# Kernel optimization log

Hardware: AMD Instinct MI355X
Metric: run time of the kernel (lower is better)

The kernel has to match this reference:

```python
import jax, jax.numpy as jnp
import numpy as np

N_NODES = 50000
N_EDGES = 800000
IN_FEATS = 128
OUT_FEATS = 64


def setup_inputs() -> dict:
    key = jax.random.key(0)
    k1, k2, k3, k4, k5, k6 = jax.random.split(key, 6)
    feat = jax.random.normal(k1, (N_NODES, IN_FEATS), dtype=jnp.float32)
    edge_src = jax.random.randint(k2, (N_EDGES,), 0, N_NODES, dtype=jnp.int64)
    edge_dst = jax.random.randint(k3, (N_EDGES,), 0, N_NODES, dtype=jnp.int64)
    eweight = jax.random.uniform(k4, (N_EDGES,), dtype=jnp.float32)
    W = jax.random.normal(k5, (OUT_FEATS, IN_FEATS), dtype=jnp.float32) * (1.0 / np.sqrt(IN_FEATS))
    b = jax.random.normal(k6, (OUT_FEATS,), dtype=jnp.float32) * 0.01
    return {"feat": feat, "edge_src": edge_src, "edge_dst": edge_dst,
            "eweight": eweight, "W": W, "b": b}


def reference(feat, edge_src, edge_dst, eweight, W, b):
    # Linear: [N, in] @ [in, out] + [out]
    h = jnp.einsum('ni,oi->no', feat, W) + b
    # u_mul_e: gather src features, scale by per-edge weight -> [E, out]
    m = h[edge_src] * eweight[:, None]
    # sum reduce over dst -> [N, out]
    out = jax.ops.segment_sum(m, edge_dst, num_segments=N_NODES)
    return out
```

## Files before the change

kernel.cpp:

```cpp
#include <hip/hip_runtime.h>

#define IN_FEATS 128
#define OUT_FEATS 64
#define TM 64
#define ALD 136
#define BW_LOG 6
#define BWIDTH 64
#define MAX_NB 1024
#define SE_PER_BLK 2048
#define CAP 2048
#define MAXR 4

typedef short bf16x8 __attribute__((ext_vector_type(8)));
typedef float f32x4 __attribute__((ext_vector_type(4)));

__device__ inline unsigned short f2bf(float f) {
    unsigned u = __float_as_uint(f);
    u += 0x7FFFu + ((u >> 16) & 1u);
    return (unsigned short)(u >> 16);
}
__device__ inline float bf2f_lo(unsigned v) { return __uint_as_float(v << 16); }
__device__ inline float bf2f_hi(unsigned v) { return __uint_as_float(v & 0xFFFF0000u); }
__device__ inline ushort4 cvt4(float4 t) {
    ushort4 s; s.x = f2bf(t.x); s.y = f2bf(t.y); s.z = f2bf(t.z); s.w = f2bf(t.w);
    return s;
}

__global__ __launch_bounds__(256) void init_cursors(int* __restrict__ gcur, int nb)
{
    for (int i = threadIdx.x; i < nb; i += 256) gcur[i] = 0;
}

__global__ __launch_bounds__(256) void stage_linear(
    const float* __restrict__ feat, const float* __restrict__ W,
    const float* __restrict__ b, unsigned short* __restrict__ h,
    const int* __restrict__ esrc, const int* __restrict__ edst,
    const float* __restrict__ ew, int* __restrict__ gcur,
    int2* __restrict__ gstage, int n_nodes, int n_edges, int nb, int nstage)
{
    __shared__ union {
        struct { unsigned short Ws[OUT_FEATS * ALD]; } lin;
        struct { int cnt[MAX_NB]; int base[MAX_NB]; } st;
    } sm;
    const int tid = threadIdx.x;

    if ((int)blockIdx.x < nstage) {
        int* cnt  = sm.st.cnt;
        int* base = sm.st.base;
        for (int i = tid; i < nb; i += 256) cnt[i] = 0;
        __syncthreads();

        const int e0 = blockIdx.x * SE_PER_BLK + tid * 8;
        int dk[8]; int sk[8]; float wk[8]; int bk[8]; int rk[8];
        if (e0 + 7 < n_edges) {
            *((int4*)&dk[0]) = *((const int4*)&edst[e0]);
            *((int4*)&dk[4]) = *((const int4*)&edst[e0 + 4]);
            *((int4*)&sk[0]) = *((const int4*)&esrc[e0]);
            *((int4*)&sk[4]) = *((const int4*)&esrc[e0 + 4]);
            *((float4*)&wk[0]) = *((const float4*)&ew[e0]);
            *((float4*)&wk[4]) = *((const float4*)&ew[e0 + 4]);
#pragma unroll
            for (int i = 0; i < 8; ++i) {
                bk[i] = dk[i] >> BW_LOG;
                rk[i] = atomicAdd(&cnt[bk[i]], 1);
            }
        } else {
#pragma unroll
            for (int i = 0; i < 8; ++i) {
                int e = e0 + i;
                if (e < n_edges) {
                    dk[i] = edst[e]; sk[i] = esrc[e]; wk[i] = ew[e];
                    bk[i] = dk[i] >> BW_LOG;
                    rk[i] = atomicAdd(&cnt[bk[i]], 1);
                } else bk[i] = -1;
            }
        }
        __syncthreads();
        for (int i = tid; i < nb; i += 256) {
            int c = cnt[i];
            base[i] = c ? atomicAdd(&gcur[i], c) : 0;
        }
        __syncthreads();
#pragma unroll
        for (int i = 0; i < 8; ++i) {
            if (bk[i] >= 0) {
                int off = base[bk[i]] + rk[i];
                if (off < CAP)
                    gstage[bk[i] * CAP + off] =
                        make_int2(((dk[i] & (BWIDTH - 1)) << 16) | sk[i],
                                  __float_as_int(wk[i]));
            }
        }
    } else {
        unsigned short* Ws = sm.lin.Ws;
        const int row0 = ((int)blockIdx.x - nstage) * TM;

        {
            const int c  = tid & 63;
            const int kb = (tid >> 6) * 32;
            const float4* wrow = (const float4*)(W + (size_t)c * IN_FEATS + kb);
#pragma unroll
            for (int i = 0; i < 8; ++i)
                *((ushort4*)&Ws[c * ALD + kb + i * 4]) = cvt4(wrow[i]);
        }
        __syncthreads();

        const int w    = tid >> 6;
        const int lane = tid & 63;
        const int m    = lane & 15;
        const int quad = lane >> 4;
        const int koff = quad * 8;

        const int gr = row0 + w * 16 + m;
        const bool rv = gr < n_nodes;
        const float* arow = feat + (size_t)gr * IN_FEATS;

        bf16x8 af[4];
        if (rv) {
            float4 t[8];
#pragma unroll
            for (int c = 0; c < 4; ++c) {
                t[2 * c]     = *((const float4*)(arow + c * 32 + koff));
                t[2 * c + 1] = *((const float4*)(arow + c * 32 + koff + 4));
            }
#pragma unroll
            for (int c = 0; c < 4; ++c) {
                ushort4 s0 = cvt4(t[2 * c]);
                ushort4 s1 = cvt4(t[2 * c + 1]);
                af[c] = (bf16x8){(short)s0.x, (short)s0.y, (short)s0.z, (short)s0.w,
                                 (short)s1.x, (short)s1.y, (short)s1.z, (short)s1.w};
            }
        } else {
#pragma unroll
            for (int c = 0; c < 4; ++c)
                af[c] = (bf16x8){0, 0, 0, 0, 0, 0, 0, 0};
        }

        f32x4 acc[4];
#pragma unroll
        for (int t = 0; t < 4; ++t) acc[t] = (f32x4){0.f, 0.f, 0.f, 0.f};

#pragma unroll
        for (int chunk = 0; chunk < 4; ++chunk) {
            const int kc = chunk * 32 + koff;
#pragma unroll
            for (int t = 0; t < 4; ++t) {
                bf16x8 bfr = *((const bf16x8*)&Ws[(t * 16 + m) * ALD + kc]);
                acc[t] = __builtin_amdgcn_mfma_f32_16x16x32_bf16(af[chunk], bfr, acc[t], 0, 0, 0);
            }
        }

#pragma unroll
        for (int t = 0; t < 4; ++t) {
            const int col = t * 16 + m;
            const float bias = b[col];
#pragma unroll
            for (int i = 0; i < 4; ++i) {
                int r = row0 + w * 16 + quad * 4 + i;
                if (r < n_nodes)
                    h[(size_t)r * OUT_FEATS + col] = f2bf(acc[t][i] + bias);
            }
        }
    }
}

__global__ __launch_bounds__(512) void sort_gather(
    const unsigned short* __restrict__ h, const int* __restrict__ gcnt,
    const int2* __restrict__ gstage, float* __restrict__ out, int n_nodes)
{
    __shared__ int2 srec[CAP];
    __shared__ int cnt[BWIDTH];
    __shared__ int cur0[BWIDTH];
    __shared__ int cur[BWIDTH];
    const int tid = threadIdx.x;
    const int b   = blockIdx.x;
    const int s0  = b * CAP;
    const int m   = min(gcnt[b], CAP);

    if (tid < BWIDTH) cnt[tid] = 0;
    __syncthreads();

    int2 rl[MAXR];
#pragma unroll
    for (int k = 0; k < MAXR; ++k) {
        int i = tid + k * 512;
        if (i < m) {
            rl[k] = gstage[s0 + i];
            atomicAdd(&cnt[(rl[k].x >> 16) & 63], 1);
        }
    }
    __syncthreads();

    if (tid < 64) {
        int v = cnt[tid];
        int inc = v;
        for (int o = 1; o < 64; o <<= 1) {
            int t = __shfl_up(inc, o, 64);
            if (tid >= o) inc += t;
        }
        int excl = inc - v;
        cur0[tid] = excl;
        cur[tid]  = excl;
    }
    __syncthreads();

#pragma unroll
    for (int k = 0; k < MAXR; ++k) {
        int i = tid + k * 512;
        if (i < m) {
            int pos = atomicAdd(&cur[(rl[k].x >> 16) & 63], 1);
            srec[pos] = rl[k];
        }
    }
    __syncthreads();

    const int lane = tid & 63;
    const int wv   = tid >> 6;
    const int g    = lane >> 4;
    const int f4   = lane & 15;
    const uint2* h64 = (const uint2*)h;

    for (int nl8 = 0; nl8 < 8; ++nl8) {
        const int nl   = wv * 8 + nl8;
        const int node = b * BWIDTH + nl;
        const int st   = cur0[nl];
        const int len  = cnt[nl];

        float a0 = 0.f, a1 = 0.f, a2 = 0.f, a3 = 0.f;
        int u = g;
        for (; u + 12 < len; u += 16) {
            int2 r0 = srec[st + u];
            int2 r1 = srec[st + u + 4];
            int2 r2 = srec[st + u + 8];
            int2 r3 = srec[st + u + 12];
            uint2 v0 = h64[(size_t)(r0.x & 0xFFFF) * 16 + f4];
            uint2 v1 = h64[(size_t)(r1.x & 0xFFFF) * 16 + f4];
            uint2 v2 = h64[(size_t)(r2.x & 0xFFFF) * 16 + f4];
            uint2 v3 = h64[(size_t)(r3.x & 0xFFFF) * 16 + f4];
            float w0 = __int_as_float(r0.y);
            float w1 = __int_as_float(r1.y);
            float w2 = __int_as_float(r2.y);
            float w3 = __int_as_float(r3.y);
            a0 += w0 * bf2f_lo(v0.x); a1 += w0 * bf2f_hi(v0.x);
            a2 += w0 * bf2f_lo(v0.y); a3 += w0 * bf2f_hi(v0.y);
            a0 += w1 * bf2f_lo(v1.x); a1 += w1 * bf2f_hi(v1.x);
            a2 += w1 * bf2f_lo(v1.y); a3 += w1 * bf2f_hi(v1.y);
            a0 += w2 * bf2f_lo(v2.x); a1 += w2 * bf2f_hi(v2.x);
            a2 += w2 * bf2f_lo(v2.y); a3 += w2 * bf2f_hi(v2.y);
            a0 += w3 * bf2f_lo(v3.x); a1 += w3 * bf2f_hi(v3.x);
            a2 += w3 * bf2f_lo(v3.y); a3 += w3 * bf2f_hi(v3.y);
        }
        for (; u + 4 < len; u += 8) {
            int2 r0 = srec[st + u];
            int2 r1 = srec[st + u + 4];
            uint2 v0 = h64[(size_t)(r0.x & 0xFFFF) * 16 + f4];
            uint2 v1 = h64[(size_t)(r1.x & 0xFFFF) * 16 + f4];
            float w0 = __int_as_float(r0.y);
            float w1 = __int_as_float(r1.y);
            a0 += w0 * bf2f_lo(v0.x); a1 += w0 * bf2f_hi(v0.x);
            a2 += w0 * bf2f_lo(v0.y); a3 += w0 * bf2f_hi(v0.y);
            a0 += w1 * bf2f_lo(v1.x); a1 += w1 * bf2f_hi(v1.x);
            a2 += w1 * bf2f_lo(v1.y); a3 += w1 * bf2f_hi(v1.y);
        }
        if (u < len) {
            int2 r = srec[st + u];
            uint2 v = h64[(size_t)(r.x & 0xFFFF) * 16 + f4];
            float w = __int_as_float(r.y);
            a0 += w * bf2f_lo(v.x); a1 += w * bf2f_hi(v.x);
            a2 += w * bf2f_lo(v.y); a3 += w * bf2f_hi(v.y);
        }
        a0 += __shfl_xor(a0, 16, 64); a0 += __shfl_xor(a0, 32, 64);
        a1 += __shfl_xor(a1, 16, 64); a1 += __shfl_xor(a1, 32, 64);
        a2 += __shfl_xor(a2, 16, 64); a2 += __shfl_xor(a2, 32, 64);
        a3 += __shfl_xor(a3, 16, 64); a3 += __shfl_xor(a3, 32, 64);

        if (g == 0 && node < n_nodes) {
            float4 o; o.x = a0; o.y = a1; o.z = a2; o.w = a3;
            *((float4*)&out[(size_t)node * OUT_FEATS + f4 * 4]) = o;
        }
    }
}

__global__ __launch_bounds__(256) void scatter_kernel(
    const unsigned short* __restrict__ h, const int* __restrict__ esrc,
    const int* __restrict__ edst, const float* __restrict__ ew,
    float* __restrict__ out, int n_edges)
{
    const int lane = threadIdx.x & 63;
    const int wave = threadIdx.x >> 6;
    const int stride = gridDim.x * 4;
    for (int e = blockIdx.x * 4 + wave; e < n_edges; e += stride) {
        const int s = esrc[e];
        const int d = edst[e];
        const float w = ew[e];
        atomicAdd(out + (size_t)d * OUT_FEATS + lane,
                  bf2f_lo((unsigned)h[(size_t)s * OUT_FEATS + lane]) * w);
    }
}

extern "C" void kernel_launch(void* const* d_in, const int* in_sizes, int n_in,
                              void* d_out, int out_size, void* d_ws, size_t ws_size,
                              hipStream_t stream) {
    const float* feat = (const float*)d_in[0];
    const int*   esrc = (const int*)d_in[1];
    const int*   edst = (const int*)d_in[2];
    const float* ew   = (const float*)d_in[3];
    const float* W    = (const float*)d_in[4];
    const float* b    = (const float*)d_in[5];
    float* out = (float*)d_out;

    const int n_nodes = in_sizes[0] / IN_FEATS;
    const int n_edges = in_sizes[1];
    const int nb = (n_nodes + BWIDTH - 1) >> BW_LOG;
    const int nlin = (n_nodes + TM - 1) / TM;
    const int nstage = (n_edges + SE_PER_BLK - 1) / SE_PER_BLK;

    char* wsb = (char*)d_ws;
    unsigned short* h = (unsigned short*)wsb;
    size_t off_gcur  = (((size_t)n_nodes * OUT_FEATS * sizeof(unsigned short)) + 15) & ~(size_t)15;
    size_t sz_gcur   = (((size_t)nb * sizeof(int)) + 15) & ~(size_t)15;
    size_t off_stage = off_gcur + sz_gcur;
    size_t needed    = off_stage + (size_t)nb * CAP * sizeof(int2);

    bool binnable = (nb <= MAX_NB) && (n_nodes < 65536) &&
                    ((size_t)n_edges / (size_t)nb * 3 / 2 + 300 <= CAP);

    if (ws_size >= needed && binnable) {
        int*  gcur   = (int*)(wsb + off_gcur);
        int2* gstage = (int2*)(wsb + off_stage);
        init_cursors<<<1, 256, 0, stream>>>(gcur, nb);
        stage_linear<<<nstage + nlin, 256, 0, stream>>>(
            feat, W, b, h, esrc, edst, ew, gcur, gstage,
            n_nodes, n_edges, nb, nstage);
        sort_gather<<<nb, 512, 0, stream>>>(h, gcur, gstage, out, n_nodes);
    } else {
        stage_linear<<<nlin, 256, 0, stream>>>(
            feat, W, b, h, esrc, edst, ew, nullptr, nullptr,
            n_nodes, n_edges, nb, 0);
        hipMemsetAsync(d_out, 0, (size_t)out_size * sizeof(float), stream);
        scatter_kernel<<<8192, 256, 0, stream>>>(h, esrc, edst, ew, out, n_edges);
    }
}
```

Baseline: 125.4 us.

## Shard per-bucket global cursors into sub-bins to cut atomic contention

```diff
diff --git a/kernel.cpp b/kernel.cpp
--- a/kernel.cpp
+++ b/kernel.cpp
@@ -8,7 +8,9 @@
 #define BWIDTH 64
 #define MAX_NB 1024
 #define SE_PER_BLK 2048
-#define CAP 2048
+#define NSH 16
+#define SUBCAP 128
+#define CAP (NSH * SUBCAP)
 #define MAXR 4
 
 typedef short bf16x8 __attribute__((ext_vector_type(8)));
@@ -26,9 +28,11 @@
     return s;
 }
 
-__global__ __launch_bounds__(256) void init_cursors(int* __restrict__ gcur, int nb)
+__global__ __launch_bounds__(256) void init_cursors(int* __restrict__ gcur, int n)
 {
-    for (int i = threadIdx.x; i < nb; i += 256) gcur[i] = 0;
+    int i = blockIdx.x * 256 + threadIdx.x;
+    int stride = gridDim.x * 256;
+    for (; i < n; i += stride) gcur[i] = 0;
 }
 
 __global__ __launch_bounds__(256) void stage_linear(
@@ -47,6 +51,7 @@
     if ((int)blockIdx.x < nstage) {
         int* cnt  = sm.st.cnt;
         int* base = sm.st.base;
+        const int sh = blockIdx.x & (NSH - 1);
         for (int i = tid; i < nb; i += 256) cnt[i] = 0;
         __syncthreads();
 
@@ -78,15 +83,15 @@
         __syncthreads();
         for (int i = tid; i < nb; i += 256) {
             int c = cnt[i];
-            base[i] = c ? atomicAdd(&gcur[i], c) : 0;
+            base[i] = c ? atomicAdd(&gcur[i * NSH + sh], c) : 0;
         }
         __syncthreads();
 #pragma unroll
         for (int i = 0; i < 8; ++i) {
             if (bk[i] >= 0) {
                 int off = base[bk[i]] + rk[i];
-                if (off < CAP)
-                    gstage[bk[i] * CAP + off] =
+                if (off < SUBCAP)
+                    gstage[bk[i] * CAP + sh * SUBCAP + off] =
                         make_int2(((dk[i] & (BWIDTH - 1)) << 16) | sk[i],
                                   __float_as_int(wk[i]));
             }
@@ -172,20 +177,25 @@
     __shared__ int cnt[BWIDTH];
     __shared__ int cur0[BWIDTH];
     __shared__ int cur[BWIDTH];
+    __shared__ int scnt[NSH];
     const int tid = threadIdx.x;
     const int b   = blockIdx.x;
-    const int s0  = b * CAP;
-    const int m   = min(gcnt[b], CAP);
-
+
+    if (tid < NSH) scnt[tid] = min(gcnt[b * NSH + tid], SUBCAP);
     if (tid < BWIDTH) cnt[tid] = 0;
     __syncthreads();
 
+    const int sh  = tid >> 5;
+    const int l32 = tid & 31;
+    const int sb  = b * CAP + sh * SUBCAP;
+    const int cs  = scnt[sh];
+
     int2 rl[MAXR];
 #pragma unroll
     for (int k = 0; k < MAXR; ++k) {
-        int i = tid + k * 512;
-        if (i < m) {
-            rl[k] = gstage[s0 + i];
+        int i = l32 + k * 32;
+        if (i < cs) {
+            rl[k] = gstage[sb + i];
             atomicAdd(&cnt[(rl[k].x >> 16) & 63], 1);
         }
     }
@@ -206,8 +216,8 @@
 
 #pragma unroll
     for (int k = 0; k < MAXR; ++k) {
-        int i = tid + k * 512;
-        if (i < m) {
+        int i = l32 + k * 32;
+        if (i < cs) {
             int pos = atomicAdd(&cur[(rl[k].x >> 16) & 63], 1);
             srec[pos] = rl[k];
         }
@@ -318,17 +328,18 @@
     char* wsb = (char*)d_ws;
     unsigned short* h = (unsigned short*)wsb;
     size_t off_gcur  = (((size_t)n_nodes * OUT_FEATS * sizeof(unsigned short)) + 15) & ~(size_t)15;
-    size_t sz_gcur   = (((size_t)nb * sizeof(int)) + 15) & ~(size_t)15;
+    size_t sz_gcur   = (((size_t)nb * NSH * sizeof(int)) + 15) & ~(size_t)15;
     size_t off_stage = off_gcur + sz_gcur;
     size_t needed    = off_stage + (size_t)nb * CAP * sizeof(int2);
 
+    size_t mean_s = (size_t)n_edges / ((size_t)nb * NSH);
     bool binnable = (nb <= MAX_NB) && (n_nodes < 65536) &&
-                    ((size_t)n_edges / (size_t)nb * 3 / 2 + 300 <= CAP);
+                    (mean_s * 2 <= SUBCAP);
 
     if (ws_size >= needed && binnable) {
         int*  gcur   = (int*)(wsb + off_gcur);
         int2* gstage = (int2*)(wsb + off_stage);
-        init_cursors<<<1, 256, 0, stream>>>(gcur, nb);
+        init_cursors<<<8, 256, 0, stream>>>(gcur, nb * NSH);
         stage_linear<<<nstage + nlin, 256, 0, stream>>>(
             feat, W, b, h, esrc, edst, ew, gcur, gstage,
             n_nodes, n_edges, nb, nstage);
```

Result: slower. 128.0 us (+2.1%).

## Fuse init, staging, linear and gather into one cooperative persistent kernel

Applied to the files above, without the earlier changes.

```diff
diff --git a/kernel.cpp b/kernel.cpp
--- a/kernel.cpp
+++ b/kernel.cpp
@@ -1,15 +1,20 @@
 #include <hip/hip_runtime.h>
+#include <hip/hip_cooperative_groups.h>
+
+namespace cg = cooperative_groups;
 
 #define IN_FEATS 128
 #define OUT_FEATS 64
 #define TM 64
+#define TMF 128
 #define ALD 136
 #define BW_LOG 6
 #define BWIDTH 64
 #define MAX_NB 1024
 #define SE_PER_BLK 2048
-#define CAP 2048
-#define MAXR 4
+#define CAP 1536
+#define MAXR 3
+#define NBLK 512
 
 typedef short bf16x8 __attribute__((ext_vector_type(8)));
 typedef float f32x4 __attribute__((ext_vector_type(4)));
@@ -24,6 +29,257 @@
 __device__ inline ushort4 cvt4(float4 t) {
     ushort4 s; s.x = f2bf(t.x); s.y = f2bf(t.y); s.z = f2bf(t.z); s.w = f2bf(t.w);
     return s;
+}
+
+__global__ __launch_bounds__(512, 4) void fused_all(
+    const float* __restrict__ feat, const float* __restrict__ W,
+    const float* __restrict__ b, unsigned short* __restrict__ h,
+    const int* __restrict__ esrc, const int* __restrict__ edst,
+    const float* __restrict__ ew, int* __restrict__ gcur,
+    int2* __restrict__ gstage, float* __restrict__ out,
+    int n_nodes, int n_edges, int nb, int nstage, int nlin)
+{
+    cg::grid_group grid = cg::this_grid();
+    __shared__ union {
+        struct { unsigned short Ws[OUT_FEATS * ALD]; } lin;
+        struct { int cnt[MAX_NB]; int base[MAX_NB]; } st;
+        struct { int2 srec[CAP]; int cnt[BWIDTH]; int cur0[BWIDTH]; int cur[BWIDTH]; } ga;
+    } sm;
+    const int tid = threadIdx.x;
+
+    for (int i = blockIdx.x * 512 + tid; i < nb; i += NBLK * 512) gcur[i] = 0;
+    grid.sync();
+
+    const int ntask = nstage + nlin;
+    for (int vb = blockIdx.x; vb < ntask; vb += NBLK) {
+        __syncthreads();
+        if (vb < nstage) {
+            int* cnt  = sm.st.cnt;
+            int* base = sm.st.base;
+            for (int i = tid; i < nb; i += 512) cnt[i] = 0;
+            __syncthreads();
+
+            const int e0 = vb * SE_PER_BLK + tid * 4;
+            int dk[4]; int sk[4]; float wk[4]; int bk[4]; int rk[4];
+            if (e0 + 3 < n_edges) {
+                *((int4*)&dk[0])   = *((const int4*)&edst[e0]);
+                *((int4*)&sk[0])   = *((const int4*)&esrc[e0]);
+                *((float4*)&wk[0]) = *((const float4*)&ew[e0]);
+#pragma unroll
+                for (int i = 0; i < 4; ++i) {
+                    bk[i] = dk[i] >> BW_LOG;
+                    rk[i] = atomicAdd(&cnt[bk[i]], 1);
+                }
+            } else {
+#pragma unroll
+                for (int i = 0; i < 4; ++i) {
+                    int e = e0 + i;
+                    if (e < n_edges) {
+                        dk[i] = edst[e]; sk[i] = esrc[e]; wk[i] = ew[e];
+                        bk[i] = dk[i] >> BW_LOG;
+                        rk[i] = atomicAdd(&cnt[bk[i]], 1);
+                    } else bk[i] = -1;
+                }
+            }
+            __syncthreads();
+            for (int i = tid; i < nb; i += 512) {
+                int c = cnt[i];
+                base[i] = c ? atomicAdd(&gcur[i], c) : 0;
+            }
+            __syncthreads();
+#pragma unroll
+            for (int i = 0; i < 4; ++i) {
+                if (bk[i] >= 0) {
+                    int off = base[bk[i]] + rk[i];
+                    if (off < CAP)
+                        gstage[bk[i] * CAP + off] =
+                            make_int2(((dk[i] & (BWIDTH - 1)) << 16) | sk[i],
+                                      __float_as_int(wk[i]));
+                }
+            }
+        } else {
+            unsigned short* Ws = sm.lin.Ws;
+            const int row0 = (vb - nstage) * TMF;
+
+            {
+                const int c  = tid & 63;
+                const int kb = (tid >> 6) * 16;
+                const float4* wrow = (const float4*)(W + (size_t)c * IN_FEATS + kb);
+#pragma unroll
+                for (int j = 0; j < 4; ++j)
+                    *((ushort4*)&Ws[c * ALD + kb + j * 4]) = cvt4(wrow[j]);
+            }
+            __syncthreads();
+
+            const int w    = tid >> 6;
+            const int lane = tid & 63;
+            const int m    = lane & 15;
+            const int quad = lane >> 4;
+            const int koff = quad * 8;
+
+            const int gr = row0 + w * 16 + m;
+            const bool rv = gr < n_nodes;
+            const float* arow = feat + (size_t)gr * IN_FEATS;
+
+            bf16x8 af[4];
+            if (rv) {
+                float4 t[8];
+#pragma unroll
+                for (int c = 0; c < 4; ++c) {
+                    t[2 * c]     = *((const float4*)(arow + c * 32 + koff));
+                    t[2 * c + 1] = *((const float4*)(arow + c * 32 + koff + 4));
+                }
+#pragma unroll
+                for (int c = 0; c < 4; ++c) {
+                    ushort4 s0 = cvt4(t[2 * c]);
+                    ushort4 s1 = cvt4(t[2 * c + 1]);
+                    af[c] = (bf16x8){(short)s0.x, (short)s0.y, (short)s0.z, (short)s0.w,
+                                     (short)s1.x, (short)s1.y, (short)s1.z, (short)s1.w};
+                }
+            } else {
+#pragma unroll
+                for (int c = 0; c < 4; ++c)
+                    af[c] = (bf16x8){0, 0, 0, 0, 0, 0, 0, 0};
+            }
+
+            f32x4 acc[4];
+#pragma unroll
+            for (int t = 0; t < 4; ++t) acc[t] = (f32x4){0.f, 0.f, 0.f, 0.f};
+
+#pragma unroll
+            for (int chunk = 0; chunk < 4; ++chunk) {
+                const int kc = chunk * 32 + koff;
+#pragma unroll
+                for (int t = 0; t < 4; ++t) {
+                    bf16x8 bfr = *((const bf16x8*)&Ws[(t * 16 + m) * ALD + kc]);
+                    acc[t] = __builtin_amdgcn_mfma_f32_16x16x32_bf16(af[chunk], bfr, acc[t], 0, 0, 0);
+                }
+            }
+
+#pragma unroll
+            for (int t = 0; t < 4; ++t) {
+                const int col = t * 16 + m;
+                const float bias = b[col];
+#pragma unroll
+                for (int i = 0; i < 4; ++i) {
+                    int r = row0 + w * 16 + quad * 4 + i;
+                    if (r < n_nodes)
+                        h[(size_t)r * OUT_FEATS + col] = f2bf(acc[t][i] + bias);
+                }
+            }
+        }
+    }
+
+    __threadfence();
+    grid.sync();
+
+    const int lane = tid & 63;
+    const int wv   = tid >> 6;
+    const int g    = lane >> 4;
+    const int f4   = lane & 15;
+    const uint2* h64 = (const uint2*)h;
+
+    for (int vb = blockIdx.x; vb < nb; vb += NBLK) {
+        __syncthreads();
+        const int s0 = vb * CAP;
+        const int m  = min(gcur[vb], CAP);
+
+        if (tid < BWIDTH) sm.ga.cnt[tid] = 0;
+        __syncthreads();
+
+        int2 rl[MAXR];
+#pragma unroll
+        for (int k = 0; k < MAXR; ++k) {
+            int i = tid + k * 512;
+            if (i < m) {
+                rl[k] = gstage[s0 + i];
+                atomicAdd(&sm.ga.cnt[(rl[k].x >> 16) & 63], 1);
+            }
+        }
+        __syncthreads();
+
+        if (tid < 64) {
+            int v = sm.ga.cnt[tid];
+            int inc = v;
+            for (int o = 1; o < 64; o <<= 1) {
+                int t = __shfl_up(inc, o, 64);
+                if (tid >= o) inc += t;
+            }
+            sm.ga.cur0[tid] = inc - v;
+            sm.ga.cur[tid]  = inc - v;
+        }
+        __syncthreads();
+
+#pragma unroll
+        for (int k = 0; k < MAXR; ++k) {
+            int i = tid + k * 512;
+            if (i < m) {
+                int pos = atomicAdd(&sm.ga.cur[(rl[k].x >> 16) & 63], 1);
+                sm.ga.srec[pos] = rl[k];
+            }
+        }
+        __syncthreads();
+
+        for (int nl8 = 0; nl8 < 8; ++nl8) {
+            const int nl   = wv * 8 + nl8;
+            const int node = vb * BWIDTH + nl;
+            const int st   = sm.ga.cur0[nl];
+            const int len  = sm.ga.cnt[nl];
+
+            float a0 = 0.f, a1 = 0.f, a2 = 0.f, a3 = 0.f;
+            int u = g;
+            for (; u + 12 < len; u += 16) {
+                int2 r0 = sm.ga.srec[st + u];
+                int2 r1 = sm.ga.srec[st + u + 4];
+                int2 r2 = sm.ga.srec[st + u + 8];
+                int2 r3 = sm.ga.srec[st + u + 12];
+                uint2 v0 = h64[(size_t)(r0.x & 0xFFFF) * 16 + f4];
+                uint2 v1 = h64[(size_t)(r1.x & 0xFFFF) * 16 + f4];
+                uint2 v2 = h64[(size_t)(r2.x & 0xFFFF) * 16 + f4];
+                uint2 v3 = h64[(size_t)(r3.x & 0xFFFF) * 16 + f4];
+                float w0 = __int_as_float(r0.y);
+                float w1 = __int_as_float(r1.y);
+                float w2 = __int_as_float(r2.y);
+                float w3 = __int_as_float(r3.y);
+                a0 += w0 * bf2f_lo(v0.x); a1 += w0 * bf2f_hi(v0.x);
+                a2 += w0 * bf2f_lo(v0.y); a3 += w0 * bf2f_hi(v0.y);
+                a0 += w1 * bf2f_lo(v1.x); a1 += w1 * bf2f_hi(v1.x);
+                a2 += w1 * bf2f_lo(v1.y); a3 += w1 * bf2f_hi(v1.y);
+                a0 += w2 * bf2f_lo(v2.x); a1 += w2 * bf2f_hi(v2.x);
+                a2 += w2 * bf2f_lo(v2.y); a3 += w2 * bf2f_hi(v2.y);
+                a0 += w3 * bf2f_lo(v3.x); a1 += w3 * bf2f_hi(v3.x);
+                a2 += w3 * bf2f_lo(v3.y); a3 += w3 * bf2f_hi(v3.y);
+            }
+            for (; u + 4 < len; u += 8) {
+                int2 r0 = sm.ga.srec[st + u];
+                int2 r1 = sm.ga.srec[st + u + 4];
+                uint2 v0 = h64[(size_t)(r0.x & 0xFFFF) * 16 + f4];
+                uint2 v1 = h64[(size_t)(r1.x & 0xFFFF) * 16 + f4];
+                float w0 = __int_as_float(r0.y);
+                float w1 = __int_as_float(r1.y);
+                a0 += w0 * bf2f_lo(v0.x); a1 += w0 * bf2f_hi(v0.x);
+                a2 += w0 * bf2f_lo(v0.y); a3 += w0 * bf2f_hi(v0.y);
+                a0 += w1 * bf2f_lo(v1.x); a1 += w1 * bf2f_hi(v1.x);
+                a2 += w1 * bf2f_lo(v1.y); a3 += w1 * bf2f_hi(v1.y);
+            }
+            if (u < len) {
+                int2 r = sm.ga.srec[st + u];
+                uint2 v = h64[(size_t)(r.x & 0xFFFF) * 16 + f4];
+                float w = __int_as_float(r.y);
+                a0 += w * bf2f_lo(v.x); a1 += w * bf2f_hi(v.x);
+                a2 += w * bf2f_lo(v.y); a3 += w * bf2f_hi(v.y);
+            }
+            a0 += __shfl_xor(a0, 16, 64); a0 += __shfl_xor(a0, 32, 64);
+            a1 += __shfl_xor(a1, 16, 64); a1 += __shfl_xor(a1, 32, 64);
+            a2 += __shfl_xor(a2, 16, 64); a2 += __shfl_xor(a2, 32, 64);
+            a3 += __shfl_xor(a3, 16, 64); a3 += __shfl_xor(a3, 32, 64);
+
+            if (g == 0 && node < n_nodes) {
+                float4 o; o.x = a0; o.y = a1; o.z = a2; o.w = a3;
+                *((float4*)&out[(size_t)node * OUT_FEATS + f4 * 4]) = o;
+            }
+        }
+    }
 }
 
 __global__ __launch_bounds__(256) void init_cursors(int* __restrict__ gcur, int nb)
@@ -94,7 +350,6 @@
     } else {
         unsigned short* Ws = sm.lin.Ws;
         const int row0 = ((int)blockIdx.x - nstage) * TM;
-
         {
             const int c  = tid & 63;
             const int kb = (tid >> 6) * 32;
@@ -110,7 +365,6 @@
         const int m    = lane & 15;
         const int quad = lane >> 4;
         const int koff = quad * 8;
-
         const int gr = row0 + w * 16 + m;
         const bool rv = gr < n_nodes;
         const float* arow = feat + (size_t)gr * IN_FEATS;
@@ -139,7 +393,6 @@
         f32x4 acc[4];
 #pragma unroll
         for (int t = 0; t < 4; ++t) acc[t] = (f32x4){0.f, 0.f, 0.f, 0.f};
-
 #pragma unroll
         for (int chunk = 0; chunk < 4; ++chunk) {
             const int kc = chunk * 32 + koff;
@@ -149,7 +402,6 @@
                 acc[t] = __builtin_amdgcn_mfma_f32_16x16x32_bf16(af[chunk], bfr, acc[t], 0, 0, 0);
             }
         }
-
 #pragma unroll
         for (int t = 0; t < 4; ++t) {
             const int col = t * 16 + m;
@@ -198,9 +450,8 @@
             int t = __shfl_up(inc, o, 64);
             if (tid >= o) inc += t;
         }
-        int excl = inc - v;
-        cur0[tid] = excl;
-        cur[tid]  = excl;
+        cur0[tid] = inc - v;
+        cur[tid]  = inc - v;
     }
     __syncthreads();
 
@@ -228,28 +479,6 @@
 
         float a0 = 0.f, a1 = 0.f, a2 = 0.f, a3 = 0.f;
         int u = g;
-        for (; u + 12 < len; u += 16) {
-            int2 r0 = srec[st + u];
-            int2 r1 = srec[st + u + 4];
-            int2 r2 = srec[st + u + 8];
-            int2 r3 = srec[st + u + 12];
-            uint2 v0 = h64[(size_t)(r0.x & 0xFFFF) * 16 + f4];
-            uint2 v1 = h64[(size_t)(r1.x & 0xFFFF) * 16 + f4];
-            uint2 v2 = h64[(size_t)(r2.x & 0xFFFF) * 16 + f4];
-            uint2 v3 = h64[(size_t)(r3.x & 0xFFFF) * 16 + f4];
-            float w0 = __int_as_float(r0.y);
-            float w1 = __int_as_float(r1.y);
-            float w2 = __int_as_float(r2.y);
-            float w3 = __int_as_float(r3.y);
-            a0 += w0 * bf2f_lo(v0.x); a1 += w0 * bf2f_hi(v0.x);
-            a2 += w0 * bf2f_lo(v0.y); a3 += w0 * bf2f_hi(v0.y);
-            a0 += w1 * bf2f_lo(v1.x); a1 += w1 * bf2f_hi(v1.x);
-            a2 += w1 * bf2f_lo(v1.y); a3 += w1 * bf2f_hi(v1.y);
-            a0 += w2 * bf2f_lo(v2.x); a1 += w2 * bf2f_hi(v2.x);
-            a2 += w2 * bf2f_lo(v2.y); a3 += w2 * bf2f_hi(v2.y);
-            a0 += w3 * bf2f_lo(v3.x); a1 += w3 * bf2f_hi(v3.x);
-            a2 += w3 * bf2f_lo(v3.y); a3 += w3 * bf2f_hi(v3.y);
-        }
         for (; u + 4 < len; u += 8) {
             int2 r0 = srec[st + u];
             int2 r1 = srec[st + u + 4];
@@ -309,11 +538,12 @@
     const float* b    = (const float*)d_in[5];
     float* out = (float*)d_out;
 
-    const int n_nodes = in_sizes[0] / IN_FEATS;
-    const int n_edges = in_sizes[1];
-    const int nb = (n_nodes + BWIDTH - 1) >> BW_LOG;
-    const int nlin = (n_nodes + TM - 1) / TM;
-    const int nstage = (n_edges + SE_PER_BLK - 1) / SE_PER_BLK;
+    int n_nodes = in_sizes[0] / IN_FEATS;
+    int n_edges = in_sizes[1];
+    int nb = (n_nodes + BWIDTH - 1) >> BW_LOG;
+    int nstage = (n_edges + SE_PER_BLK - 1) / SE_PER_BLK;
+    int nlin_f = (n_nodes + TMF - 1) / TMF;
+    int nlin   = (n_nodes + TM - 1) / TM;
 
     char* wsb = (char*)d_ws;
     unsigned short* h = (unsigned short*)wsb;
@@ -322,17 +552,28 @@
     size_t off_stage = off_gcur + sz_gcur;
     size_t needed    = off_stage + (size_t)nb * CAP * sizeof(int2);
 
+    double mean = (double)n_edges / (double)nb;
     bool binnable = (nb <= MAX_NB) && (n_nodes < 65536) &&
-                    ((size_t)n_edges / (size_t)nb * 3 / 2 + 300 <= CAP);
+                    (mean + 8.0 * __builtin_sqrt(mean) + 64.0 <= (double)CAP);
 
     if (ws_size >= needed && binnable) {
         int*  gcur   = (int*)(wsb + off_gcur);
         int2* gstage = (int2*)(wsb + off_stage);
-        init_cursors<<<1, 256, 0, stream>>>(gcur, nb);
-        stage_linear<<<nstage + nlin, 256, 0, stream>>>(
-            feat, W, b, h, esrc, edst, ew, gcur, gstage,
-            n_nodes, n_edges, nb, nstage);
-        sort_gather<<<nb, 512, 0, stream>>>(h, gcur, gstage, out, n_nodes);
+
+        void* args[] = { (void*)&feat, (void*)&W, (void*)&b, (void*)&h,
+                         (void*)&esrc, (void*)&edst, (void*)&ew,
+                         (void*)&gcur, (void*)&gstage, (void*)&out,
+                         (void*)&n_nodes, (void*)&n_edges, (void*)&nb,
+                         (void*)&nstage, (void*)&nlin_f };
+        hipError_t err = hipLaunchCooperativeKernel(
+            (const void*)fused_all, dim3(NBLK), dim3(512), args, 0, stream);
+        if (err != hipSuccess) {
+            init_cursors<<<1, 256, 0, stream>>>(gcur, nb);
+            stage_linear<<<nstage + nlin, 256, 0, stream>>>(
+                feat, W, b, h, esrc, edst, ew, gcur, gstage,
+                n_nodes, n_edges, nb, nstage);
+            sort_gather<<<nb, 512, 0, stream>>>(h, gcur, gstage, out, n_nodes);
+        }
     } else {
         stage_linear<<<nlin, 256, 0, stream>>>(
             feat, W, b, h, esrc, edst, ew, nullptr, nullptr,
```

New measurement: 353.0 us. 2.82x slower.

## Replace global atomic bucket cursors with per-block fixed-slot staging runs

Applied to the files above, without the earlier changes.

```diff
diff --git a/kernel.cpp b/kernel.cpp
--- a/kernel.cpp
+++ b/kernel.cpp
@@ -8,8 +8,8 @@
 #define BWIDTH 64
 #define MAX_NB 1024
 #define SE_PER_BLK 2048
-#define CAP 2048
-#define MAXR 4
+#define SLOTS 24
+#define CAPG 1536
 
 typedef short bf16x8 __attribute__((ext_vector_type(8)));
 typedef float f32x4 __attribute__((ext_vector_type(4)));
@@ -26,28 +26,22 @@
     return s;
 }
 
-__global__ __launch_bounds__(256) void init_cursors(int* __restrict__ gcur, int nb)
-{
-    for (int i = threadIdx.x; i < nb; i += 256) gcur[i] = 0;
-}
-
 __global__ __launch_bounds__(256) void stage_linear(
     const float* __restrict__ feat, const float* __restrict__ W,
     const float* __restrict__ b, unsigned short* __restrict__ h,
     const int* __restrict__ esrc, const int* __restrict__ edst,
-    const float* __restrict__ ew, int* __restrict__ gcur,
+    const float* __restrict__ ew, int* __restrict__ cnts,
     int2* __restrict__ gstage, int n_nodes, int n_edges, int nb, int nstage)
 {
     __shared__ union {
         struct { unsigned short Ws[OUT_FEATS * ALD]; } lin;
-        struct { int cnt[MAX_NB]; int base[MAX_NB]; } st;
+        struct { int cur[MAX_NB]; } st;
     } sm;
     const int tid = threadIdx.x;
 
     if ((int)blockIdx.x < nstage) {
-        int* cnt  = sm.st.cnt;
-        int* base = sm.st.base;
-        for (int i = tid; i < nb; i += 256) cnt[i] = 0;
+        int* cur = sm.st.cur;
+        for (int i = tid; i < nb; i += 256) cur[i] = 0;
         __syncthreads();
 
         const int e0 = blockIdx.x * SE_PER_BLK + tid * 8;
@@ -62,7 +56,7 @@
 #pragma unroll
             for (int i = 0; i < 8; ++i) {
                 bk[i] = dk[i] >> BW_LOG;
-                rk[i] = atomicAdd(&cnt[bk[i]], 1);
+                rk[i] = atomicAdd(&cur[bk[i]], 1);
             }
         } else {
 #pragma unroll
@@ -71,26 +65,21 @@
                 if (e < n_edges) {
                     dk[i] = edst[e]; sk[i] = esrc[e]; wk[i] = ew[e];
                     bk[i] = dk[i] >> BW_LOG;
-                    rk[i] = atomicAdd(&cnt[bk[i]], 1);
+                    rk[i] = atomicAdd(&cur[bk[i]], 1);
                 } else bk[i] = -1;
             }
         }
+#pragma unroll
+        for (int i = 0; i < 8; ++i) {
+            if (bk[i] >= 0 && rk[i] < SLOTS) {
+                gstage[((size_t)bk[i] * nstage + blockIdx.x) * SLOTS + rk[i]] =
+                    make_int2(((dk[i] & (BWIDTH - 1)) << 16) | sk[i],
+                              __float_as_int(wk[i]));
+            }
+        }
         __syncthreads();
-        for (int i = tid; i < nb; i += 256) {
-            int c = cnt[i];
-            base[i] = c ? atomicAdd(&gcur[i], c) : 0;
-        }
-        __syncthreads();
-#pragma unroll
-        for (int i = 0; i < 8; ++i) {
-            if (bk[i] >= 0) {
-                int off = base[bk[i]] + rk[i];
-                if (off < CAP)
-                    gstage[bk[i] * CAP + off] =
-                        make_int2(((dk[i] & (BWIDTH - 1)) << 16) | sk[i],
-                                  __float_as_int(wk[i]));
-            }
-        }
+        for (int i = tid; i < nb; i += 256)
+            cnts[(size_t)blockIdx.x * nb + i] = min(cur[i], SLOTS);
     } else {
         unsigned short* Ws = sm.lin.Ws;
         const int row0 = ((int)blockIdx.x - nstage) * TM;
@@ -165,29 +154,26 @@
 }
 
 __global__ __launch_bounds__(512) void sort_gather(
-    const unsigned short* __restrict__ h, const int* __restrict__ gcnt,
-    const int2* __restrict__ gstage, float* __restrict__ out, int n_nodes)
+    const unsigned short* __restrict__ h, const int* __restrict__ cnts,
+    const int2* __restrict__ gstage, float* __restrict__ out,
+    int n_nodes, int nb, int nstage)
 {
-    __shared__ int2 srec[CAP];
+    __shared__ int2 srec[CAPG];
     __shared__ int cnt[BWIDTH];
     __shared__ int cur0[BWIDTH];
     __shared__ int cur[BWIDTH];
     const int tid = threadIdx.x;
     const int b   = blockIdx.x;
-    const int s0  = b * CAP;
-    const int m   = min(gcnt[b], CAP);
-
+
+    int c_r = 0;
+    if (tid < nstage) c_r = cnts[(size_t)tid * nb + b];
     if (tid < BWIDTH) cnt[tid] = 0;
     __syncthreads();
 
-    int2 rl[MAXR];
-#pragma unroll
-    for (int k = 0; k < MAXR; ++k) {
-        int i = tid + k * 512;
-        if (i < m) {
-            rl[k] = gstage[s0 + i];
-            atomicAdd(&cnt[(rl[k].x >> 16) & 63], 1);
-        }
+    const int2* run = gstage + ((size_t)b * nstage + tid) * SLOTS;
+    for (int j = 0; j < c_r; ++j) {
+        int2 r = run[j];
+        atomicAdd(&cnt[(r.x >> 16) & 63], 1);
     }
     __syncthreads();
 
@@ -198,19 +184,15 @@
             int t = __shfl_up(inc, o, 64);
             if (tid >= o) inc += t;
         }
-        int excl = inc - v;
-        cur0[tid] = excl;
-        cur[tid]  = excl;
+        cur0[tid] = inc - v;
+        cur[tid]  = inc - v;
     }
     __syncthreads();
 
-#pragma unroll
-    for (int k = 0; k < MAXR; ++k) {
-        int i = tid + k * 512;
-        if (i < m) {
-            int pos = atomicAdd(&cur[(rl[k].x >> 16) & 63], 1);
-            srec[pos] = rl[k];
-        }
+    for (int j = 0; j < c_r; ++j) {
+        int2 r = run[j];
+        int pos = atomicAdd(&cur[(r.x >> 16) & 63], 1);
+        if (pos < CAPG) srec[pos] = r;
     }
     __syncthreads();
 
@@ -224,32 +206,11 @@
         const int nl   = wv * 8 + nl8;
         const int node = b * BWIDTH + nl;
         const int st   = cur0[nl];
-        const int len  = cnt[nl];
+        int len        = cnt[nl];
+        len = (st < CAPG) ? min(len, CAPG - st) : 0;
 
         float a0 = 0.f, a1 = 0.f, a2 = 0.f, a3 = 0.f;
         int u = g;
-        for (; u + 12 < len; u += 16) {
-            int2 r0 = srec[st + u];
-            int2 r1 = srec[st + u + 4];
-            int2 r2 = srec[st + u + 8];
-            int2 r3 = srec[st + u + 12];
-            uint2 v0 = h64[(size_t)(r0.x & 0xFFFF) * 16 + f4];
-            uint2 v1 = h64[(size_t)(r1.x & 0xFFFF) * 16 + f4];
-            uint2 v2 = h64[(size_t)(r2.x & 0xFFFF) * 16 + f4];
-            uint2 v3 = h64[(size_t)(r3.x & 0xFFFF) * 16 + f4];
-            float w0 = __int_as_float(r0.y);
-            float w1 = __int_as_float(r1.y);
-            float w2 = __int_as_float(r2.y);
-            float w3 = __int_as_float(r3.y);
-            a0 += w0 * bf2f_lo(v0.x); a1 += w0 * bf2f_hi(v0.x);
-            a2 += w0 * bf2f_lo(v0.y); a3 += w0 * bf2f_hi(v0.y);
-            a0 += w1 * bf2f_lo(v1.x); a1 += w1 * bf2f_hi(v1.x);
-            a2 += w1 * bf2f_lo(v1.y); a3 += w1 * bf2f_hi(v1.y);
-            a0 += w2 * bf2f_lo(v2.x); a1 += w2 * bf2f_hi(v2.x);
-            a2 += w2 * bf2f_lo(v2.y); a3 += w2 * bf2f_hi(v2.y);
-            a0 += w3 * bf2f_lo(v3.x); a1 += w3 * bf2f_hi(v3.x);
-            a2 += w3 * bf2f_lo(v3.y); a3 += w3 * bf2f_hi(v3.y);
-        }
         for (; u + 4 < len; u += 8) {
             int2 r0 = srec[st + u];
             int2 r1 = srec[st + u + 4];
@@ -317,22 +278,23 @@
 
     char* wsb = (char*)d_ws;
     unsigned short* h = (unsigned short*)wsb;
-    size_t off_gcur  = (((size_t)n_nodes * OUT_FEATS * sizeof(unsigned short)) + 15) & ~(size_t)15;
-    size_t sz_gcur   = (((size_t)nb * sizeof(int)) + 15) & ~(size_t)15;
-    size_t off_stage = off_gcur + sz_gcur;
-    size_t needed    = off_stage + (size_t)nb * CAP * sizeof(int2);
-
-    bool binnable = (nb <= MAX_NB) && (n_nodes < 65536) &&
-                    ((size_t)n_edges / (size_t)nb * 3 / 2 + 300 <= CAP);
+    size_t off_cnts  = (((size_t)n_nodes * OUT_FEATS * sizeof(unsigned short)) + 255) & ~(size_t)255;
+    size_t sz_cnts   = (((size_t)nstage * nb * sizeof(int)) + 255) & ~(size_t)255;
+    size_t off_stage = off_cnts + sz_cnts;
+    size_t needed    = off_stage + (size_t)nb * nstage * SLOTS * sizeof(int2);
+
+    double mean_bb = (double)SE_PER_BLK / (double)nb;
+    bool binnable = (nb <= MAX_NB) && (n_nodes < 65536) && (nstage <= 512) &&
+                    (mean_bb * 4.0 + 4.0 <= (double)SLOTS);
 
     if (ws_size >= needed && binnable) {
-        int*  gcur   = (int*)(wsb + off_gcur);
+        int*  cnts   = (int*)(wsb + off_cnts);
         int2* gstage = (int2*)(wsb + off_stage);
-        init_cursors<<<1, 256, 0, stream>>>(gcur, nb);
         stage_linear<<<nstage + nlin, 256, 0, stream>>>(
-            feat, W, b, h, esrc, edst, ew, gcur, gstage,
+            feat, W, b, h, esrc, edst, ew, cnts, gstage,
             n_nodes, n_edges, nb, nstage);
-        sort_gather<<<nb, 512, 0, stream>>>(h, gcur, gstage, out, n_nodes);
+        sort_gather<<<nb, 512, 0, stream>>>(h, cnts, gstage, out,
+                                            n_nodes, nb, nstage);
     } else {
         stage_linear<<<nlin, 256, 0, stream>>>(
             feat, W, b, h, esrc, edst, ew, nullptr, nullptr,
```

New measurement: 133.3 us. 1.06x slower.
